# Optimization experiments

Hardware: AMD Instinct MI355X
Metric: run time of the kernel (lower is better)

## Reference

```python
import jax, jax.numpy as jnp
import numpy as np

# 5-tap image-gradient filter (cross-correlation taps, as in F.conv2d)
_K5 = (-1.0 / 12.0, 2.0 / 3.0, 0.0, -2.0 / 3.0, 1.0 / 12.0)
ALPHA = BETA = GAMMA = DELTA = 1.0
MASK_COST = 1.0
ENTROPY_WEIGHT = 1.0


def _pen(x):
    return jnp.sqrt(x + 1e-5)


def _filt_w(x):
    # depthwise 1x5 filter along W, padding 2 (matches F.conv2d(x, kernel_gx, padding=(0,2)))
    W = x.shape[-1]
    xp = jnp.pad(x, ((0, 0), (0, 0), (0, 0), (2, 2)))
    out = _K5[0] * xp[..., 0:W]
    for j in range(1, 5):
        out = out + _K5[j] * xp[..., j:j + W]
    return out


def _filt_h(x):
    # depthwise 5x1 filter along H, padding 2
    H = x.shape[-2]
    xp = jnp.pad(x, ((0, 0), (0, 0), (2, 2), (0, 0)))
    out = _K5[0] * xp[..., 0:H, :]
    for j in range(1, 5):
        out = out + _K5[j] * xp[..., j:j + H, :]
    return out


def _warp(img, flow):
    # Bilinear warp: sample img at (x + flow_x, y + flow_y); out-of-range taps contribute 0
    B, C, H, W = img.shape
    xq = jnp.arange(W, dtype=img.dtype)[None, None, :] + flow[:, 0]  # (B,H,W)
    yq = jnp.arange(H, dtype=img.dtype)[None, :, None] + flow[:, 1]
    x0 = jnp.floor(xq)
    y0 = jnp.floor(yq)
    wx1 = xq - x0
    wy1 = yq - y0
    img_flat = img.reshape(B, C, H * W)

    def tap(xi, yi, w):
        valid = (xi >= 0) & (xi <= W - 1) & (yi >= 0) & (yi <= H - 1)
        xc = jnp.clip(xi, 0, W - 1).astype(jnp.int32)
        yc = jnp.clip(yi, 0, H - 1).astype(jnp.int32)
        idx = (yc * W + xc).reshape(B, 1, H * W)
        vals = jnp.take_along_axis(img_flat, jnp.broadcast_to(idx, (B, C, H * W)), axis=2)
        vals = vals.reshape(B, C, H, W)
        return vals * (w * valid.astype(img.dtype))[:, None]

    return (tap(x0, y0, (1 - wx1) * (1 - wy1)) + tap(x0 + 1, y0, wx1 * (1 - wy1))
            + tap(x0, y0 + 1, (1 - wx1) * wy1) + tap(x0 + 1, y0 + 1, wx1 * wy1))


def _border_mask(flow):
    B, _, H, W = flow.shape
    Xp = jnp.arange(W, dtype=flow.dtype)[None, None, :] + flow[:, 0]
    Yp = jnp.arange(H, dtype=flow.dtype)[None, :, None] + flow[:, 1]
    mask_x = jax.nn.sigmoid(Xp + 0.5) * (1.0 - jax.nn.sigmoid(Xp - (W - 0.5)))
    mask_y = jax.nn.sigmoid(Yp + 0.5) * (1.0 - jax.nn.sigmoid(Yp - (H - 0.5)))
    return mask_x * mask_y


def _direction_terms(flow_a, flow_b, img_a, img_b):
    # energy terms for one direction (warping *_b by flow_a)
    mask = _border_mask(flow_a)
    flow_b_warp = _warp(flow_b, flow_a)
    mag = jnp.sum(flow_a ** 2 + flow_b_warp ** 2, axis=1)
    diff = flow_a + flow_b_warp
    occ = 1.0 - jax.nn.sigmoid(jnp.sum(diff ** 2, axis=1) - (0.01 * mag + 0.5))
    mask = mask * occ
    mask_term = MASK_COST * jnp.sum(1.0 - mask, axis=(1, 2)).mean()
    img_b_warp = _warp(img_b, flow_a)
    A = jnp.sum((img_a - img_b_warp) ** 2, axis=1)
    data_term = ALPHA * jnp.sum(_pen(A) * mask, axis=(1, 2)).mean()
    dx = flow_a[..., 1:] - flow_a[..., :-1]
    dy = flow_a[:, :, 1:, :] - flow_a[:, :, :-1, :]
    Bt = (jnp.pad(jnp.sum(dx ** 2, axis=1), ((0, 0), (0, 0), (0, 1)))
          + jnp.pad(jnp.sum(dy ** 2, axis=1), ((0, 0), (0, 1), (0, 0))))
    smooth_term = BETA * jnp.sum(_pen(Bt), axis=(1, 2)).mean()
    Ct = (jnp.sum((_filt_w(img_a) - _filt_w(img_b_warp)) ** 2, axis=1)
          + jnp.sum((_filt_h(img_a) - _filt_h(img_b_warp)) ** 2, axis=1))
    grad_term = GAMMA * jnp.sum(_pen(Ct) * mask, axis=(1, 2)).mean()
    D = jnp.sum(diff ** 2, axis=1)
    fb_part = DELTA * jnp.sum(_pen(D) * mask, axis=(1, 2)).mean()
    return mask_term + data_term + smooth_term + grad_term + fb_part


def _elbo_epe(meanf, log_varf, meanb, log_varb, img1, img2, target, noise_f, noise_b):
    # reparameterized flow samples (Nsamples = 1)
    flowf = meanf + jnp.exp(log_varf / 2.0) * noise_f
    flowb = meanb + jnp.exp(log_varb / 2.0) * noise_b
    energy = (_direction_terms(flowf, flowb, img1, img2)
              + _direction_terms(flowb, flowf, img2, img1))
    entropy = (jnp.sum(log_varf, axis=(1, 2, 3)) / 2
               + jnp.sum(log_varb, axis=(1, 2, 3)) / 2).mean()
    elbo = energy - ENTROPY_WEIGHT * entropy
    epe = jnp.sqrt(jnp.sum((meanf - target) ** 2, axis=1)).mean()
    return elbo, epe


def setup_inputs() -> dict:
    key = jax.random.key(0)
    ks = jax.random.split(key, 9)
    B, H, W = 8, 384, 512
    return {
        "meanf": jax.random.normal(ks[0], (B, 2, H, W), jnp.float32),
        "log_varf": jax.random.normal(ks[1], (B, 2, H, W), jnp.float32),
        "meanb": jax.random.normal(ks[2], (B, 2, H, W), jnp.float32),
        "log_varb": jax.random.normal(ks[3], (B, 2, H, W), jnp.float32),
        "img1": jax.random.uniform(ks[4], (B, 3, H, W), jnp.float32),
        "img2": jax.random.uniform(ks[5], (B, 3, H, W), jnp.float32),
        "target": jax.random.normal(ks[6], (B, 2, H, W), jnp.float32),
        "noise_f": jax.random.normal(ks[7], (B, 2, H, W), jnp.float32),
        "noise_b": jax.random.normal(ks[8], (B, 2, H, W), jnp.float32),
    }


def reference(meanf, log_varf, meanb, log_varb, img1, img2, target, noise_f, noise_b):
    elbo, epe = _elbo_epe(meanf, log_varf, meanb, log_varb, img1, img2, target, noise_f, noise_b)
    return (elbo, epe)
```

## Files before the change

### kernel.cpp

```cpp
#include <hip/hip_runtime.h>
#include <math.h>

#define BATCH 8
#define IH 384
#define IW 512
#define NPIX (IH*IW)
#define BN (BATCH*NPIX)

#define TW 64
#define TH 16
#define RW (TW+4)
#define RH (TH+4)
#define NTX (IW/TW)
#define NTY (IH/TH)
#define NZ  (BATCH*2)
#define NB_DIR (NTX*NTY*NZ)

#define HSX 8
#define HSY 6
#define SH (TH+2*HSY)
#define SW (TW+2*HSX)
#define SF4 (SW/4)

#define NITER_A 4

#define NB_FLOW 1536
#define PA_OFF 0
#define PB_OFF NB_DIR
#define ENT_OFF (2*NB_DIR)
#define EPE_OFF (ENT_OFF + NB_FLOW)
#define PART_FLOATS 16384

__device__ __forceinline__ float frcp_(float x){ return __builtin_amdgcn_rcpf(x); }
__device__ __forceinline__ float fsqrt_(float x){ return __builtin_amdgcn_sqrtf(x); }
__device__ __forceinline__ float sigmoidf_(float x){ return frcp_(1.0f + __expf(-x)); }

__device__ __forceinline__ float block_reduce_sum(float v){
    __shared__ float s[8];
    #pragma unroll
    for (int off=32; off>0; off>>=1) v += __shfl_down(v, off);
    int lane = threadIdx.x & 63, wid = threadIdx.x >> 6;
    if (lane==0) s[wid] = v;
    __syncthreads();
    float t = 0.f;
    if (wid==0){
        int nw = (blockDim.x+63)>>6;
        t = (lane < nw) ? s[lane] : 0.f;
        #pragma unroll
        for (int off=4; off>0; off>>=1) t += __shfl_down(t, off);
    }
    __syncthreads();
    return t;
}

__global__ __launch_bounds__(256)
void flows_kernel(const float* __restrict__ meanf, const float* __restrict__ log_varf,
                  const float* __restrict__ meanb, const float* __restrict__ log_varb,
                  const float* __restrict__ target,
                  const float* __restrict__ noise_f, const float* __restrict__ noise_b,
                  float* __restrict__ flowf, float* __restrict__ flowb,
                  float* __restrict__ part)
{
    int t = blockIdx.x*blockDim.x + threadIdx.x;
    if (t < NB_DIR) part[PB_OFF + t] = 0.f;
    const int NP4 = NPIX/4;
    int b = t / NP4, p4 = t - b*NP4;
    size_t i0 = ((size_t)b*2*NPIX)/4 + p4;
    size_t i1 = i0 + NPIX/4;

    const float4* mf = (const float4*)meanf;  const float4* lf = (const float4*)log_varf;
    const float4* mb = (const float4*)meanb;  const float4* lb = (const float4*)log_varb;
    const float4* nf = (const float4*)noise_f; const float4* nb = (const float4*)noise_b;
    const float4* tg = (const float4*)target;
    float4* ff = (float4*)flowf; float4* fbp = (float4*)flowb;

    float4 lf0 = lf[i0], lf1 = lf[i1], lb0 = lb[i0], lb1 = lb[i1];
    float4 mf0 = mf[i0], mf1 = mf[i1], mb0 = mb[i0], mb1 = mb[i1];
    float4 nf0 = nf[i0], nf1 = nf[i1], nb0 = nb[i0], nb1 = nb[i1];

    float4 of0, of1;
    of0.x = mf0.x + __expf(0.5f*lf0.x)*nf0.x; of0.y = mf0.y + __expf(0.5f*lf0.y)*nf0.y;
    of0.z = mf0.z + __expf(0.5f*lf0.z)*nf0.z; of0.w = mf0.w + __expf(0.5f*lf0.w)*nf0.w;
    of1.x = mf1.x + __expf(0.5f*lf1.x)*nf1.x; of1.y = mf1.y + __expf(0.5f*lf1.y)*nf1.y;
    of1.z = mf1.z + __expf(0.5f*lf1.z)*nf1.z; of1.w = mf1.w + __expf(0.5f*lf1.w)*nf1.w;
    float4 ob0, ob1;
    ob0.x = mb0.x + __expf(0.5f*lb0.x)*nb0.x; ob0.y = mb0.y + __expf(0.5f*lb0.y)*nb0.y;
    ob0.z = mb0.z + __expf(0.5f*lb0.z)*nb0.z; ob0.w = mb0.w + __expf(0.5f*lb0.w)*nb0.w;
    ob1.x = mb1.x + __expf(0.5f*lb1.x)*nb1.x; ob1.y = mb1.y + __expf(0.5f*lb1.y)*nb1.y;
    ob1.z = mb1.z + __expf(0.5f*lb1.z)*nb1.z; ob1.w = mb1.w + __expf(0.5f*lb1.w)*nb1.w;

    size_t o4 = (size_t)b*(NPIX/2) + (size_t)p4*2;
    float4 v;
    v.x = of0.x; v.y = of1.x; v.z = of0.y; v.w = of1.y; ff[o4]   = v;
    v.x = of0.z; v.y = of1.z; v.z = of0.w; v.w = of1.w; ff[o4+1] = v;
    v.x = ob0.x; v.y = ob1.x; v.z = ob0.y; v.w = ob1.y; fbp[o4]   = v;
    v.x = ob0.z; v.y = ob1.z; v.z = ob0.w; v.w = ob1.w; fbp[o4+1] = v;

    float ent = (lf0.x+lf0.y+lf0.z+lf0.w) + (lf1.x+lf1.y+lf1.z+lf1.w)
              + (lb0.x+lb0.y+lb0.z+lb0.w) + (lb1.x+lb1.y+lb1.z+lb1.w);

    float4 t0 = tg[i0], t1 = tg[i1];
    float d0, d1, epe = 0.f;
    d0 = mf0.x - t0.x; d1 = mf1.x - t1.x; epe += fsqrt_(d0*d0 + d1*d1);
    d0 = mf0.y - t0.y; d1 = mf1.y - t1.y; epe += fsqrt_(d0*d0 + d1*d1);
    d0 = mf0.z - t0.z; d1 = mf1.z - t1.z; epe += fsqrt_(d0*d0 + d1*d1);
    d0 = mf0.w - t0.w; d1 = mf1.w - t1.w; epe += fsqrt_(d0*d0 + d1*d1);

    float s = block_reduce_sum(ent);
    if (threadIdx.x == 0) part[ENT_OFF + blockIdx.x] = s;
    float s2 = block_reduce_sum(epe);
    if (threadIdx.x == 0) part[EPE_OFF + blockIdx.x] = s2;
}

__global__ __launch_bounds__(256, 6)
void dirA_kernel(const float* __restrict__ flowf, const float* __restrict__ flowb,
                 const float* __restrict__ img1, const float* __restrict__ img2,
                 float* __restrict__ wimg, float* __restrict__ maskbuf,
                 float* __restrict__ part)
{
    __shared__ float sib[3][SH][SW];

    const int z = blockIdx.z;
    const int dir = z & 1, b = z >> 1;
    const float2 *pfa2, *pfb2;
    const float *pia, *pib;
    if (dir == 0){
        pfa2 = (const float2*)flowf + (size_t)b*NPIX;
        pfb2 = (const float2*)flowb + (size_t)b*NPIX;
        pia = img1 + (size_t)b*3*NPIX; pib = img2 + (size_t)b*3*NPIX;
    } else {
        pfa2 = (const float2*)flowb + (size_t)b*NPIX;
        pfb2 = (const float2*)flowf + (size_t)b*NPIX;
        pia = img2 + (size_t)b*3*NPIX; pib = img1 + (size_t)b*3*NPIX;
    }

    float* wout = wimg + (size_t)z*3*NPIX;
    float* mout = maskbuf + (size_t)z*NPIX;

    const int tw0 = blockIdx.x*TW, th0 = blockIdx.y*TH;
    const int tid = threadIdx.x;
    float local = 0.f;

    for (int i = tid; i < 3*SH*SF4; i += 256){
        int c = i / (SH*SF4);
        int rem = i - c*(SH*SF4);
        int r = rem / SF4, c4 = rem - r*SF4;
        int gy = th0 - HSY + r;
        int gx = tw0 - HSX + 4*c4;
        float4 v = make_float4(0.f, 0.f, 0.f, 0.f);
        if (gy >= 0 && gy < IH && gx >= 0 && gx < IW){
            v = *(const float4*)(pib + (size_t)c*NPIX + gy*IW + gx);
        }
        *(float4*)&sib[c][r][4*c4] = v;
    }

    float2 rfa[NITER_A];
    #pragma unroll
    for (int it = 0; it < NITER_A; ++it){
        int i = tid + it*256;
        int hh = i >> 6, ww = i & 63;
        int p = (th0 + hh)*IW + (tw0 + ww);
        rfa[it] = pfa2[p];
    }
    __syncthreads();

    #pragma unroll
    for (int it = 0; it < NITER_A; ++it){
        int i = tid + it*256;
        int hh = i >> 6, ww = i & 63;
        int gh = th0 + hh, gw = tw0 + ww;
        int p = gh*IW + gw;
        float fax = rfa[it].x, fay = rfa[it].y;
        float Xp = (float)gw + fax;
        float Yp = (float)gh + fay;

        float2 f_r = (gw < IW-1) ? pfa2[p+1]  : make_float2(0.f, 0.f);
        float2 f_d = (gh < IH-1) ? pfa2[p+IW] : make_float2(0.f, 0.f);

        float x0f = floorf(Xp), y0f = floorf(Yp);
        float wx1 = Xp - x0f, wy1 = Yp - y0f;
        float wx0 = 1.f - wx1, wy0 = 1.f - wy1;

        float x1f = x0f + 1.f, y1f = y0f + 1.f;
        bool vx0 = (x0f >= 0.f) && (x0f <= (float)(IW-1));
        bool vx1 = (x1f >= 0.f) && (x1f <= (float)(IW-1));
        bool vy0 = (y0f >= 0.f) && (y0f <= (float)(IH-1));
        bool vy1 = (y1f >= 0.f) && (y1f <= (float)(IH-1));
        float xc0 = fminf(fmaxf(x0f, 0.f), (float)(IW-1));
        float xc1 = fminf(fmaxf(x1f, 0.f), (float)(IW-1));
        float yc0 = fminf(fmaxf(y0f, 0.f), (float)(IH-1));
        float yc1 = fminf(fmaxf(y1f, 0.f), (float)(IH-1));
        int ix0 = (int)xc0, ix1 = (int)xc1, iy0 = (int)yc0, iy1 = (int)yc1;
        int idx0 = iy0*IW + ix0, idx1 = iy0*IW + ix1;
        int idx2 = iy1*IW + ix0, idx3 = iy1*IW + ix1;
        float wt0 = (vx0 && vy0) ? wx0*wy0 : 0.f;
        float wt1 = (vx1 && vy0) ? wx1*wy0 : 0.f;
        float wt2 = (vx0 && vy1) ? wx0*wy1 : 0.f;
        float wt3 = (vx1 && vy1) ? wx1*wy1 : 0.f;

        float2 fb0 = pfb2[idx0], fb1 = pfb2[idx1];
        float2 fb2 = pfb2[idx2], fb3 = pfb2[idx3];

        float a0 = pia[p], a1 = pia[NPIX+p], a2 = pia[2*NPIX+p];

        float w0, w1, w2;
        int lx0 = ix0 - (tw0 - HSX), ly0 = iy0 - (th0 - HSY);
        int lx1 = ix1 - (tw0 - HSX), ly1 = iy1 - (th0 - HSY);
        bool inwin = (lx0 >= 0) && (lx1 < SW) && (ly0 >= 0) && (ly1 < SH);
        if (inwin){
            int o00 = ly0*SW + lx0, o01 = ly0*SW + lx1;
            int o10 = ly1*SW + lx0, o11 = ly1*SW + lx1;
            const float* s0 = &sib[0][0][0];
            const float* s1 = s0 + SH*SW;
            const float* s2 = s1 + SH*SW;
            w0 = wt0*s0[o00] + wt1*s0[o01] + wt2*s0[o10] + wt3*s0[o11];
            w1 = wt0*s1[o00] + wt1*s1[o01] + wt2*s1[o10] + wt3*s1[o11];
            w2 = wt0*s2[o00] + wt1*s2[o01] + wt2*s2[o10] + wt3*s2[o11];
        } else {
            const float* g1 = pib + NPIX;
            const float* g2 = pib + 2*NPIX;
            w0 = wt0*pib[idx0] + wt1*pib[idx1] + wt2*pib[idx2] + wt3*pib[idx3];
            w1 = wt0*g1[idx0]  + wt1*g1[idx1]  + wt2*g1[idx2]  + wt3*g1[idx3];
            w2 = wt0*g2[idx0]  + wt1*g2[idx1]  + wt2*g2[idx2]  + wt3*g2[idx3];
        }

        float mx = sigmoidf_(Xp + 0.5f) * (1.f - sigmoidf_(Xp - ((float)IW - 0.5f)));
        float my = sigmoidf_(Yp + 0.5f) * (1.f - sigmoidf_(Yp - ((float)IH - 0.5f)));
        float bm = mx * my;

        float fbwx = wt0*fb0.x + wt1*fb1.x + wt2*fb2.x + wt3*fb3.x;
        float fbwy = wt0*fb0.y + wt1*fb1.y + wt2*fb2.y + wt3*fb3.y;

        float mag = fax*fax + fay*fay + fbwx*fbwx + fbwy*fbwy;
        float dfx = fax + fbwx, dfy = fay + fbwy;
        float D = dfx*dfx + dfy*dfy;
        float occ = 1.f - sigmoidf_(D - (0.01f*mag + 0.5f));
        float mask = bm * occ;

        local += (1.f - mask);

        float d0 = a0 - w0;
        float d1 = a1 - w1;
        float d2 = a2 - w2;
        local += fsqrt_(d0*d0 + d1*d1 + d2*d2 + 1e-5f) * mask;

        local += fsqrt_(D + 1e-5f) * mask;

        float Bt = 0.f;
        if (gw < IW-1){
            float e0 = f_r.x - fax;
            float e1 = f_r.y - fay;
            Bt += e0*e0 + e1*e1;
        }
        if (gh < IH-1){
            float e0 = f_d.x - fax;
            float e1 = f_d.y - fay;
            Bt += e0*e0 + e1*e1;
        }
        local += fsqrt_(Bt + 1e-5f);

        wout[p]          = w0;
        wout[NPIX + p]   = w1;
        wout[2*NPIX + p] = w2;
        mout[p]          = mask;
    }

    float s = block_reduce_sum(local);
    if (tid == 0) part[PA_OFF + blockIdx.x + NTX*(blockIdx.y + NTY*blockIdx.z)] = s;
}

__global__ __launch_bounds__(256, 4)
void dirB_kernel(const float* __restrict__ img1, const float* __restrict__ img2,
                 const float* __restrict__ wimg, const float* __restrict__ maskbuf,
                 float* __restrict__ part)
{
    __shared__ float wt[3][RH][RW];
    __shared__ float at[3][RH][RW];

    const int z = blockIdx.z;
    const int dir = z & 1, b = z >> 1;
    const float* pia = ((dir == 0) ? img1 : img2) + (size_t)b*3*NPIX;
    const float* wsrc = wimg + (size_t)z*3*NPIX;
    const float* msrc = maskbuf + (size_t)z*NPIX;

    const int tw0 = blockIdx.x*TW, th0 = blockIdx.y*TH;
    const int tid = threadIdx.x;
    float local = 0.f;

    for (int i = tid; i < 3*RH*RW; i += 256){
        int c = i / (RH*RW);
        int rem = i - c*(RH*RW);
        int r = rem / RW, cc = rem - r*RW;
        int gy = th0 + r - 2;
        int gx = tw0 + cc - 2;
        float va = 0.f, vw = 0.f;
        if (gy >= 0 && gy < IH && gx >= 0 && gx < IW){
            size_t q = (size_t)c*NPIX + gy*IW + gx;
            va = pia[q];
            vw = wsrc[q];
        }
        at[c][r][cc] = va;
        wt[c][r][cc] = vw;
    }
    __syncthreads();

    const float K0 = -1.f/12.f, K1 = 2.f/3.f, K3 = -2.f/3.f, K4 = 1.f/12.f;
    #pragma unroll
    for (int it = 0; it < NITER_A; ++it){
        int i = tid + it*256;
        int hh = i >> 6, ww = i & 63;
        int p = (th0 + hh)*IW + (tw0 + ww);
        int lh = hh + 2, lw = ww + 2;
        float Ct = 0.f;
        #pragma unroll
        for (int c = 0; c < 3; ++c){
            float gxa = K0*at[c][lh][lw-2] + K1*at[c][lh][lw-1]
                      + K3*at[c][lh][lw+1] + K4*at[c][lh][lw+2];
            float gxw = K0*wt[c][lh][lw-2] + K1*wt[c][lh][lw-1]
                      + K3*wt[c][lh][lw+1] + K4*wt[c][lh][lw+2];
            float d = gxa - gxw; Ct += d*d;
            float gya = K0*at[c][lh-2][lw] + K1*at[c][lh-1][lw]
                      + K3*at[c][lh+1][lw] + K4*at[c][lh+2][lw];
            float gyw = K0*wt[c][lh-2][lw] + K1*wt[c][lh-1][lw]
                      + K3*wt[c][lh+1][lw] + K4*wt[c][lh+2][lw];
            d = gya - gyw; Ct += d*d;
        }
        local += fsqrt_(Ct + 1e-5f) * msrc[p];
    }

    float s = block_reduce_sum(local);
    if (tid == 0) part[PB_OFF + blockIdx.x + NTX*(blockIdx.y + NTY*blockIdx.z)] = s;
}

__global__ __launch_bounds__(256)
void finalize_kernel(const float* __restrict__ part, float* __restrict__ out)
{
    float e = 0.f, ent = 0.f, epe = 0.f;
    for (int i = threadIdx.x; i < 2*NB_DIR; i += 256) e += part[i];
    for (int i = threadIdx.x; i < NB_FLOW; i += 256){
        ent += part[ENT_OFF + i];
        epe += part[EPE_OFF + i];
    }
    e   = block_reduce_sum(e);
    ent = block_reduce_sum(ent);
    epe = block_reduce_sum(epe);
    if (threadIdx.x == 0){
        out[0] = e / (float)BATCH - ent / (2.f * (float)BATCH);
        out[1] = epe / ((float)BATCH * (float)NPIX);
    }
}

extern "C" void kernel_launch(void* const* d_in, const int* in_sizes, int n_in,
                              void* d_out, int out_size, void* d_ws, size_t ws_size,
                              hipStream_t stream)
{
    const float* meanf    = (const float*)d_in[0];
    const float* log_varf = (const float*)d_in[1];
    const float* meanb    = (const float*)d_in[2];
    const float* log_varb = (const float*)d_in[3];
    const float* img1     = (const float*)d_in[4];
    const float* img2     = (const float*)d_in[5];
    const float* target   = (const float*)d_in[6];
    const float* noise_f  = (const float*)d_in[7];
    const float* noise_b  = (const float*)d_in[8];

    float* ws    = (float*)d_ws;
    float* part  = ws;
    float* flowf = ws + PART_FLOATS;
    float* flowb = flowf + 2*(size_t)BN;
    float* wimg  = flowb + 2*(size_t)BN;
    float* maskb = wimg + (size_t)NZ*3*NPIX;

    const int threads = 256;

    flows_kernel<<<NB_FLOW, threads, 0, stream>>>(meanf, log_varf, meanb, log_varb,
                                                  target, noise_f, noise_b,
                                                  flowf, flowb, part);

    dim3 grid(NTX, NTY, NZ);
    dirA_kernel<<<grid, threads, 0, stream>>>(flowf, flowb, img1, img2,
                                              wimg, maskb, part);
    dirB_kernel<<<grid, threads, 0, stream>>>(img1, img2, wimg, maskb, part);

    finalize_kernel<<<1, threads, 0, stream>>>(part, (float*)d_out);
}
```

Measured before the change: 247.7 us.

## Switch flow to planar layout and software-pipeline backward-flow gathers in dirA

The prep kernel now writes the sampled flows in planar (x plane, y plane) layout instead of interleaved float2, and dirA reads them as separate float planes. dirA prefetches the next iteration's four backward-flow gather taps while computing the current one, to hide gather latency. Image and neighbour flow loads are moved next to their use, and dirB's launch bound goes from 4 to 5 blocks. Planar layout doubles the number of gather instructions per tap and the prefetch raises register pressure.

```diff
diff --git a/kernel.cpp b/kernel.cpp
--- a/kernel.cpp
+++ b/kernel.cpp
@@ -78,23 +78,19 @@
     float4 mf0 = mf[i0], mf1 = mf[i1], mb0 = mb[i0], mb1 = mb[i1];
     float4 nf0 = nf[i0], nf1 = nf[i1], nb0 = nb[i0], nb1 = nb[i1];
 
-    float4 of0, of1;
-    of0.x = mf0.x + __expf(0.5f*lf0.x)*nf0.x; of0.y = mf0.y + __expf(0.5f*lf0.y)*nf0.y;
-    of0.z = mf0.z + __expf(0.5f*lf0.z)*nf0.z; of0.w = mf0.w + __expf(0.5f*lf0.w)*nf0.w;
-    of1.x = mf1.x + __expf(0.5f*lf1.x)*nf1.x; of1.y = mf1.y + __expf(0.5f*lf1.y)*nf1.y;
-    of1.z = mf1.z + __expf(0.5f*lf1.z)*nf1.z; of1.w = mf1.w + __expf(0.5f*lf1.w)*nf1.w;
-    float4 ob0, ob1;
-    ob0.x = mb0.x + __expf(0.5f*lb0.x)*nb0.x; ob0.y = mb0.y + __expf(0.5f*lb0.y)*nb0.y;
-    ob0.z = mb0.z + __expf(0.5f*lb0.z)*nb0.z; ob0.w = mb0.w + __expf(0.5f*lb0.w)*nb0.w;
-    ob1.x = mb1.x + __expf(0.5f*lb1.x)*nb1.x; ob1.y = mb1.y + __expf(0.5f*lb1.y)*nb1.y;
-    ob1.z = mb1.z + __expf(0.5f*lb1.z)*nb1.z; ob1.w = mb1.w + __expf(0.5f*lb1.w)*nb1.w;
-
-    size_t o4 = (size_t)b*(NPIX/2) + (size_t)p4*2;
-    float4 v;
-    v.x = of0.x; v.y = of1.x; v.z = of0.y; v.w = of1.y; ff[o4]   = v;
-    v.x = of0.z; v.y = of1.z; v.z = of0.w; v.w = of1.w; ff[o4+1] = v;
-    v.x = ob0.x; v.y = ob1.x; v.z = ob0.y; v.w = ob1.y; fbp[o4]   = v;
-    v.x = ob0.z; v.y = ob1.z; v.z = ob0.w; v.w = ob1.w; fbp[o4+1] = v;
+    float4 o;
+    o.x = mf0.x + __expf(0.5f*lf0.x)*nf0.x; o.y = mf0.y + __expf(0.5f*lf0.y)*nf0.y;
+    o.z = mf0.z + __expf(0.5f*lf0.z)*nf0.z; o.w = mf0.w + __expf(0.5f*lf0.w)*nf0.w;
+    ff[i0] = o;
+    o.x = mf1.x + __expf(0.5f*lf1.x)*nf1.x; o.y = mf1.y + __expf(0.5f*lf1.y)*nf1.y;
+    o.z = mf1.z + __expf(0.5f*lf1.z)*nf1.z; o.w = mf1.w + __expf(0.5f*lf1.w)*nf1.w;
+    ff[i1] = o;
+    o.x = mb0.x + __expf(0.5f*lb0.x)*nb0.x; o.y = mb0.y + __expf(0.5f*lb0.y)*nb0.y;
+    o.z = mb0.z + __expf(0.5f*lb0.z)*nb0.z; o.w = mb0.w + __expf(0.5f*lb0.w)*nb0.w;
+    fbp[i0] = o;
+    o.x = mb1.x + __expf(0.5f*lb1.x)*nb1.x; o.y = mb1.y + __expf(0.5f*lb1.y)*nb1.y;
+    o.z = mb1.z + __expf(0.5f*lb1.z)*nb1.z; o.w = mb1.w + __expf(0.5f*lb1.w)*nb1.w;
+    fbp[i1] = o;
 
     float ent = (lf0.x+lf0.y+lf0.z+lf0.w) + (lf1.x+lf1.y+lf1.z+lf1.w)
               + (lb0.x+lb0.y+lb0.z+lb0.w) + (lb1.x+lb1.y+lb1.z+lb1.w);
@@ -112,6 +108,33 @@
     if (threadIdx.x == 0) part[EPE_OFF + blockIdx.x] = s2;
 }
 
+struct FB8 { float v0,v1,v2,v3,v4,v5,v6,v7; };
+
+__device__ __forceinline__ void tap_idx_(int gw, int gh, float fax, float fay,
+                                         int& idx0, int& idx1, int& idx2, int& idx3)
+{
+    float Xp = (float)gw + fax;
+    float Yp = (float)gh + fay;
+    float x0f = floorf(Xp), y0f = floorf(Yp);
+    float xc0 = fminf(fmaxf(x0f,       0.f), (float)(IW-1));
+    float xc1 = fminf(fmaxf(x0f + 1.f, 0.f), (float)(IW-1));
+    float yc0 = fminf(fmaxf(y0f,       0.f), (float)(IH-1));
+    float yc1 = fminf(fmaxf(y0f + 1.f, 0.f), (float)(IH-1));
+    int ix0 = (int)xc0, ix1 = (int)xc1, iy0 = (int)yc0, iy1 = (int)yc1;
+    idx0 = iy0*IW + ix0; idx1 = iy0*IW + ix1;
+    idx2 = iy1*IW + ix0; idx3 = iy1*IW + ix1;
+}
+
+__device__ __forceinline__ FB8 fb_load_(const float* __restrict__ pfb,
+                                        int idx0, int idx1, int idx2, int idx3)
+{
+    const float* pfb1 = pfb + NPIX;
+    FB8 r;
+    r.v0 = pfb[idx0];  r.v1 = pfb[idx1];  r.v2 = pfb[idx2];  r.v3 = pfb[idx3];
+    r.v4 = pfb1[idx0]; r.v5 = pfb1[idx1]; r.v6 = pfb1[idx2]; r.v7 = pfb1[idx3];
+    return r;
+}
+
 __global__ __launch_bounds__(256, 6)
 void dirA_kernel(const float* __restrict__ flowf, const float* __restrict__ flowb,
                  const float* __restrict__ img1, const float* __restrict__ img2,
@@ -122,23 +145,18 @@
 
     const int z = blockIdx.z;
     const int dir = z & 1, b = z >> 1;
-    const float2 *pfa2, *pfb2;
-    const float *pia, *pib;
-    if (dir == 0){
-        pfa2 = (const float2*)flowf + (size_t)b*NPIX;
-        pfb2 = (const float2*)flowb + (size_t)b*NPIX;
-        pia = img1 + (size_t)b*3*NPIX; pib = img2 + (size_t)b*3*NPIX;
-    } else {
-        pfa2 = (const float2*)flowb + (size_t)b*NPIX;
-        pfb2 = (const float2*)flowf + (size_t)b*NPIX;
-        pia = img2 + (size_t)b*3*NPIX; pib = img1 + (size_t)b*3*NPIX;
-    }
+    const float *pfa, *pfb, *pia, *pib;
+    if (dir == 0){ pfa = flowf; pfb = flowb; pia = img1; pib = img2; }
+    else         { pfa = flowb; pfb = flowf; pia = img2; pib = img1; }
+    pfa += (size_t)b*2*NPIX; pfb += (size_t)b*2*NPIX;
+    pia += (size_t)b*3*NPIX; pib += (size_t)b*3*NPIX;
 
     float* wout = wimg + (size_t)z*3*NPIX;
     float* mout = maskbuf + (size_t)z*NPIX;
 
     const int tw0 = blockIdx.x*TW, th0 = blockIdx.y*TH;
     const int tid = threadIdx.x;
+    const int hh0 = tid >> 6, ww0 = tid & 63;
     float local = 0.f;
 
     for (int i = tid; i < 3*SH*SF4; i += 256){
@@ -154,28 +172,37 @@
         *(float4*)&sib[c][r][4*c4] = v;
     }
 
-    float2 rfa[NITER_A];
+    float rfax[NITER_A], rfay[NITER_A];
     #pragma unroll
     for (int it = 0; it < NITER_A; ++it){
-        int i = tid + it*256;
-        int hh = i >> 6, ww = i & 63;
-        int p = (th0 + hh)*IW + (tw0 + ww);
-        rfa[it] = pfa2[p];
+        int p = (th0 + hh0 + it*4)*IW + (tw0 + ww0);
+        rfax[it] = pfa[p];
+        rfay[it] = pfa[NPIX + p];
     }
     __syncthreads();
+
+    FB8 fb_cur, fb_nxt;
+    {
+        int j0, j1, j2, j3;
+        tap_idx_(tw0 + ww0, th0 + hh0, rfax[0], rfay[0], j0, j1, j2, j3);
+        fb_cur = fb_load_(pfb, j0, j1, j2, j3);
+    }
 
     #pragma unroll
     for (int it = 0; it < NITER_A; ++it){
-        int i = tid + it*256;
-        int hh = i >> 6, ww = i & 63;
+        int hh = hh0 + it*4, ww = ww0;
         int gh = th0 + hh, gw = tw0 + ww;
         int p = gh*IW + gw;
-        float fax = rfa[it].x, fay = rfa[it].y;
+        float fax = rfax[it], fay = rfay[it];
+
+        if (it + 1 < NITER_A){
+            int j0, j1, j2, j3;
+            tap_idx_(gw, th0 + hh0 + (it+1)*4, rfax[it+1], rfay[it+1], j0, j1, j2, j3);
+            fb_nxt = fb_load_(pfb, j0, j1, j2, j3);
+        }
+
         float Xp = (float)gw + fax;
         float Yp = (float)gh + fay;
-
-        float2 f_r = (gw < IW-1) ? pfa2[p+1]  : make_float2(0.f, 0.f);
-        float2 f_d = (gh < IH-1) ? pfa2[p+IW] : make_float2(0.f, 0.f);
 
         float x0f = floorf(Xp), y0f = floorf(Yp);
         float wx1 = Xp - x0f, wy1 = Yp - y0f;
@@ -197,11 +224,6 @@
         float wt1 = (vx1 && vy0) ? wx1*wy0 : 0.f;
         float wt2 = (vx0 && vy1) ? wx0*wy1 : 0.f;
         float wt3 = (vx1 && vy1) ? wx1*wy1 : 0.f;
-
-        float2 fb0 = pfb2[idx0], fb1 = pfb2[idx1];
-        float2 fb2 = pfb2[idx2], fb3 = pfb2[idx3];
-
-        float a0 = pia[p], a1 = pia[NPIX+p], a2 = pia[2*NPIX+p];
 
         float w0, w1, w2;
         int lx0 = ix0 - (tw0 - HSX), ly0 = iy0 - (th0 - HSY);
@@ -228,8 +250,8 @@
         float my = sigmoidf_(Yp + 0.5f) * (1.f - sigmoidf_(Yp - ((float)IH - 0.5f)));
         float bm = mx * my;
 
-        float fbwx = wt0*fb0.x + wt1*fb1.x + wt2*fb2.x + wt3*fb3.x;
-        float fbwy = wt0*fb0.y + wt1*fb1.y + wt2*fb2.y + wt3*fb3.y;
+        float fbwx = wt0*fb_cur.v0 + wt1*fb_cur.v1 + wt2*fb_cur.v2 + wt3*fb_cur.v3;
+        float fbwy = wt0*fb_cur.v4 + wt1*fb_cur.v5 + wt2*fb_cur.v6 + wt3*fb_cur.v7;
 
         float mag = fax*fax + fay*fay + fbwx*fbwx + fbwy*fbwy;
         float dfx = fax + fbwx, dfy = fay + fbwy;
@@ -239,22 +261,22 @@
 
         local += (1.f - mask);
 
-        float d0 = a0 - w0;
-        float d1 = a1 - w1;
-        float d2 = a2 - w2;
+        float d0 = pia[p]        - w0;
+        float d1 = pia[NPIX+p]   - w1;
+        float d2 = pia[2*NPIX+p] - w2;
         local += fsqrt_(d0*d0 + d1*d1 + d2*d2 + 1e-5f) * mask;
 
         local += fsqrt_(D + 1e-5f) * mask;
 
         float Bt = 0.f;
         if (gw < IW-1){
-            float e0 = f_r.x - fax;
-            float e1 = f_r.y - fay;
+            float e0 = pfa[p+1] - fax;
+            float e1 = pfa[NPIX + p+1] - fay;
             Bt += e0*e0 + e1*e1;
         }
         if (gh < IH-1){
-            float e0 = f_d.x - fax;
-            float e1 = f_d.y - fay;
+            float e0 = pfa[p+IW] - fax;
+            float e1 = pfa[NPIX + p+IW] - fay;
             Bt += e0*e0 + e1*e1;
         }
         local += fsqrt_(Bt + 1e-5f);
@@ -263,13 +285,15 @@
         wout[NPIX + p]   = w1;
         wout[2*NPIX + p] = w2;
         mout[p]          = mask;
+
+        if (it + 1 < NITER_A) fb_cur = fb_nxt;
     }
 
     float s = block_reduce_sum(local);
     if (tid == 0) part[PA_OFF + blockIdx.x + NTX*(blockIdx.y + NTY*blockIdx.z)] = s;
 }
 
-__global__ __launch_bounds__(256, 4)
+__global__ __launch_bounds__(256, 5)
 void dirB_kernel(const float* __restrict__ img1, const float* __restrict__ img2,
                  const float* __restrict__ wimg, const float* __restrict__ maskbuf,
                  float* __restrict__ part)
```

New measurement: 256.4 us. 3.5% more time.
